# Optimization experiments

Measured on AMD Instinct MI355X. Metric: run time of the kernel, lower is better.

## Reference

```python
import jax, jax.numpy as jnp
import numpy as np

LN_EPS = 1e-5
WINDOWS = (5, 10, 20)


def _rolling_vol_mean(returns, w):
    # returns: [B, L]; rolling unbiased std (torch.std, ddof=1) over window w,
    # then mean over all window positions -> [B, 1]
    B = returns.shape[0]
    z = jnp.zeros((B, 1), returns.dtype)
    c1 = jnp.concatenate([z, jnp.cumsum(returns, axis=1)], axis=1)
    c2 = jnp.concatenate([z, jnp.cumsum(returns * returns, axis=1)], axis=1)
    s1 = c1[:, w:] - c1[:, :-w]          # window sums      [B, L-w+1]
    s2 = c2[:, w:] - c2[:, :-w]          # window sq sums   [B, L-w+1]
    var = (s2 - s1 * s1 / w) / (w - 1)
    std = jnp.sqrt(jnp.maximum(var, 0.0))
    return jnp.mean(std, axis=1, keepdims=True)


def _layernorm(x, g, b):
    mu = jnp.mean(x, axis=-1, keepdims=True)
    v = jnp.mean((x - mu) ** 2, axis=-1, keepdims=True)
    return (x - mu) / jnp.sqrt(v + LN_EPS) * g + b


def setup_inputs() -> dict:
    key = jax.random.key(0)
    ks = jax.random.split(key, 8)
    B, S, F = 4096, 4096, 1
    input_dim, hidden = 64, 256
    h2 = hidden // 2
    price_series = jax.random.uniform(ks[0], (B, S, F), jnp.float32) + 0.5
    sd = 0.02
    return {
        "price_series": price_series,
        "W1": jax.random.normal(ks[1], (input_dim, h2), jnp.float32) * sd,
        "b1": jnp.zeros((h2,), jnp.float32),
        "g1": jnp.ones((h2,), jnp.float32),
        "be1": jnp.zeros((h2,), jnp.float32),
        "W2": jax.random.normal(ks[2], (h2, h2), jnp.float32) * sd,
        "b2": jnp.zeros((h2,), jnp.float32),
        "g2": jnp.ones((h2,), jnp.float32),
        "be2": jnp.zeros((h2,), jnp.float32),
        "Wc1": jax.random.normal(ks[3], (hidden, 64), jnp.float32) * sd,
        "bc1": jnp.zeros((64,), jnp.float32),
        "Wc2": jax.random.normal(ks[4], (64, 4), jnp.float32) * sd,
        "bc2": jnp.zeros((4,), jnp.float32),
    }


def reference(price_series, W1, b1, g1, be1, W2, b2, g2, be2, Wc1, bc1, Wc2, bc2):
    input_dim = W1.shape[0]
    # features == 1 path: log returns
    safe_prices = jnp.clip(price_series, 1e-8, None)
    log_prices = jnp.log(safe_prices)
    returns = (log_prices[:, 1:, 0] - log_prices[:, :-1, 0])  # [B, S-1]

    vol_feats = [_rolling_vol_mean(returns, w) for w in WINDOWS]
    vol = jnp.concatenate(vol_feats, axis=1)                  # [B, 3]
    B = vol.shape[0]
    pad = jnp.zeros((B, input_dim - vol.shape[1]), vol.dtype)
    vol = jnp.concatenate([vol, pad], axis=1)                 # [B, input_dim]

    h = _layernorm(jax.nn.relu(vol @ W1 + b1), g1, be1)       # [B, h2]
    h2f = _layernorm(jax.nn.relu(h @ W2 + b2), g2, be2)       # [B, h2]
    combined = jnp.concatenate([h, h2f], axis=1)              # [B, hidden]
    logits = jax.nn.relu(combined @ Wc1 + bc1) @ Wc2 + bc2    # dropout = identity at eval
    regime = jax.nn.softmax(logits, axis=1)
    return combined, regime
```

## Files before the change

### kernel.cpp

```cpp
#include <hip/hip_runtime.h>
#include <math.h>

constexpr int S   = 4096;
constexpr int L   = S - 1;
constexpr int H2  = 128;
constexpr int HID = 256;
constexpr int NPOS = 16;
constexpr int WMAX = 20;
constexpr int RMAX = NPOS + WMAX - 1;
constexpr float LN_EPS = 1e-5f;

constexpr int LP4 = 1040;

__device__ __forceinline__ float fast_sqrt(float x)  { return __builtin_amdgcn_sqrtf(x); }
__device__ __forceinline__ float fast_rsqrt(float x) { return __builtin_amdgcn_rsqf(x); }

__device__ __forceinline__ int swz(int slot) { return slot ^ ((slot >> 2) & 3); }

__device__ __forceinline__ float2 block_sum2(float a, float b, int tid, float* red8) {
    #pragma unroll
    for (int off = 32; off; off >>= 1) {
        a += __shfl_down(a, off);
        b += __shfl_down(b, off);
    }
    if ((tid & 63) == 0) { red8[(tid >> 6) * 2] = a; red8[(tid >> 6) * 2 + 1] = b; }
    __syncthreads();
    float2 r = make_float2(red8[0] + red8[2] + red8[4] + red8[6],
                           red8[1] + red8[3] + red8[5] + red8[7]);
    __syncthreads();
    return r;
}

template<int W>
__device__ __forceinline__ float window_acc(const float (&rr)[RMAX], int t0,
                                            float s1, float s2) {
    constexpr float c1 = 1.f / (float)(W - 1);
    constexpr float c2 = 1.f / ((float)W * (float)(W - 1));
    const int n = L - W + 1;
    float acc = 0.f;
    #pragma unroll
    for (int i = 0; i < NPOS; ++i) {
        float t  = fmaf(-(s1 * c2), s1, s2 * c1);
        float sd = fast_sqrt(fmaxf(t, 0.f));
        if (t0 + i < n) acc += sd;
        if (i < NPOS - 1) {
            float xin = rr[i + W], xout = rr[i];
            s1 += xin; s1 -= xout;
            s2 = fmaf(xin, xin, s2);
            s2 = fmaf(-xout, xout, s2);
        }
    }
    return acc;
}

__global__ __launch_bounds__(256)
void vol_fused(const float* __restrict__ prices,
               const float* __restrict__ W1,  const float* __restrict__ b1,
               const float* __restrict__ g1,  const float* __restrict__ be1,
               const float* __restrict__ W2,  const float* __restrict__ b2,
               const float* __restrict__ g2,  const float* __restrict__ be2,
               const float* __restrict__ Wc1, const float* __restrict__ bc1,
               const float* __restrict__ Wc2, const float* __restrict__ bc2,
               float* __restrict__ out_combined, float* __restrict__ out_regime)
{
    __shared__ __align__(16) float4 lp4[LP4];
    __shared__ float redv[16];
    __shared__ float vols[4];

    float* fbuf = reinterpret_cast<float*>(lp4);
    float* comb = fbuf;
    float* part = fbuf + 256;
    float* red8 = fbuf + 1280;

    const int tid = threadIdx.x;
    const int b   = blockIdx.x;

    const float4* prow = reinterpret_cast<const float4*>(prices + (size_t)b * S);
    #pragma unroll
    for (int i = 0; i < 4; ++i) {
        int slot = tid + i * 256;
        float4 v = prow[slot];
        float4 w;
        w.x = __logf(fmaxf(v.x, 1e-8f));
        w.y = __logf(fmaxf(v.y, 1e-8f));
        w.z = __logf(fmaxf(v.z, 1e-8f));
        w.w = __logf(fmaxf(v.w, 1e-8f));
        lp4[swz(slot)] = w;
    }
    if (tid < 16) lp4[swz(1024 + tid)] = make_float4(0.f, 0.f, 0.f, 0.f);
    __syncthreads();

    const int t0 = tid * NPOS;
    const int st = tid * 4;
    float lpv[36];
    #pragma unroll
    for (int j = 0; j < 9; ++j) {
        float4 v = lp4[swz(st + j)];
        lpv[4 * j + 0] = v.x; lpv[4 * j + 1] = v.y;
        lpv[4 * j + 2] = v.z; lpv[4 * j + 3] = v.w;
    }
    float rr[RMAX];
    #pragma unroll
    for (int i = 0; i < RMAX; ++i) rr[i] = lpv[i + 1] - lpv[i];

    float s1a = 0.f, s2a = 0.f;
    #pragma unroll
    for (int j = 0; j < 5; ++j) { s1a += rr[j]; s2a = fmaf(rr[j], rr[j], s2a); }
    float s1b = s1a, s2b = s2a;
    #pragma unroll
    for (int j = 5; j < 10; ++j) { s1b += rr[j]; s2b = fmaf(rr[j], rr[j], s2b); }
    float s1c = s1b, s2c = s2b;
    #pragma unroll
    for (int j = 10; j < 20; ++j) { s1c += rr[j]; s2c = fmaf(rr[j], rr[j], s2c); }

    float sum5  = window_acc<5>(rr, t0, s1a, s2a);
    float sum10 = window_acc<10>(rr, t0, s1b, s2b);
    float sum20 = window_acc<20>(rr, t0, s1c, s2c);

    #pragma unroll
    for (int off = 32; off; off >>= 1) {
        sum5  += __shfl_down(sum5,  off);
        sum10 += __shfl_down(sum10, off);
        sum20 += __shfl_down(sum20, off);
    }
    if ((tid & 63) == 0) {
        int w = tid >> 6;
        redv[w * 3 + 0] = sum5; redv[w * 3 + 1] = sum10; redv[w * 3 + 2] = sum20;
    }
    __syncthreads();
    if (tid < 3) {
        constexpr float sc[3] = { 1.f / (L - 5 + 1), 1.f / (L - 10 + 1), 1.f / (L - 20 + 1) };
        vols[tid] = (redv[tid] + redv[3 + tid] + redv[6 + tid] + redv[9 + tid]) * sc[tid];
    }
    __syncthreads();

    const float v0 = vols[0], v1 = vols[1], v2 = vols[2];

    float x = 0.f;
    if (tid < H2) {
        x = b1[tid];
        x = fmaf(v0, W1[0 * H2 + tid], x);
        x = fmaf(v1, W1[1 * H2 + tid], x);
        x = fmaf(v2, W1[2 * H2 + tid], x);
        x = fmaxf(x, 0.f);
    }
    float2 s = block_sum2((tid < H2) ? x : 0.f, (tid < H2) ? x * x : 0.f, tid, red8);
    {
        float mu  = s.x * (1.f / H2);
        float var = s.y * (1.f / H2) - mu * mu;
        if (tid < H2)
            comb[tid] = (x - mu) * fast_rsqrt(fmaxf(var, 0.f) + LN_EPS) * g1[tid] + be1[tid];
    }
    __syncthreads();

    {
        const int q = tid & 31, seg = tid >> 5;
        const float* w2base = W2 + (size_t)(seg * 16) * H2 + q * 4;
        float ax = 0.f, ay = 0.f, az = 0.f, aw = 0.f;
        #pragma unroll
        for (int k = 0; k < 16; ++k) {
            float a = comb[seg * 16 + k];
            float4 w = *reinterpret_cast<const float4*>(w2base + (size_t)k * H2);
            ax = fmaf(a, w.x, ax); ay = fmaf(a, w.y, ay);
            az = fmaf(a, w.z, az); aw = fmaf(a, w.w, aw);
        }
        float4* p4 = reinterpret_cast<float4*>(part);
        p4[tid] = make_float4(ax, ay, az, aw);
    }
    __syncthreads();
    float x2 = 0.f;
    if (tid < H2) {
        float ssum = 0.f;
        #pragma unroll
        for (int sg = 0; sg < 8; ++sg) ssum += part[sg * 128 + tid];
        x2 = fmaxf(ssum + b2[tid], 0.f);
    }
    s = block_sum2((tid < H2) ? x2 : 0.f, (tid < H2) ? x2 * x2 : 0.f, tid, red8);
    {
        float mu  = s.x * (1.f / H2);
        float var = s.y * (1.f / H2) - mu * mu;
        if (tid < H2)
            comb[H2 + tid] = (x2 - mu) * fast_rsqrt(fmaxf(var, 0.f) + LN_EPS) * g2[tid] + be2[tid];
    }
    __syncthreads();

    out_combined[(size_t)b * HID + tid] = comb[tid];

    {
        const int q = tid & 15, seg = tid >> 4;
        const float* wcbase = Wc1 + (size_t)(seg * 16) * 64 + q * 4;
        float ax = 0.f, ay = 0.f, az = 0.f, aw = 0.f;
        #pragma unroll
        for (int k = 0; k < 16; ++k) {
            float a = comb[seg * 16 + k];
            float4 w = *reinterpret_cast<const float4*>(wcbase + (size_t)k * 64);
            ax = fmaf(a, w.x, ax); ay = fmaf(a, w.y, ay);
            az = fmaf(a, w.z, az); aw = fmaf(a, w.w, aw);
        }
        float4* p4 = reinterpret_cast<float4*>(part);
        p4[tid] = make_float4(ax, ay, az, aw);
    }
    __syncthreads();

    if (tid < 64) {
        float ssum = 0.f;
        #pragma unroll
        for (int sg = 0; sg < 16; ++sg) ssum += part[sg * 64 + tid];
        float c1 = fmaxf(ssum + bc1[tid], 0.f);

        float4 wrow = reinterpret_cast<const float4*>(Wc2)[tid];
        float lx = c1 * wrow.x, ly = c1 * wrow.y, lz = c1 * wrow.z, lw = c1 * wrow.w;
        #pragma unroll
        for (int off = 32; off; off >>= 1) {
            lx += __shfl_down(lx, off);
            ly += __shfl_down(ly, off);
            lz += __shfl_down(lz, off);
            lw += __shfl_down(lw, off);
        }
        if (tid == 0) {
            float4 bb = *reinterpret_cast<const float4*>(bc2);
            float l0 = lx + bb.x, l1 = ly + bb.y, l2 = lz + bb.z, l3 = lw + bb.w;
            float m  = fmaxf(fmaxf(l0, l1), fmaxf(l2, l3));
            float e0 = __expf(l0 - m), e1 = __expf(l1 - m);
            float e2 = __expf(l2 - m), e3 = __expf(l3 - m);
            float inv = 1.f / (e0 + e1 + e2 + e3);
            reinterpret_cast<float4*>(out_regime)[b] =
                make_float4(e0 * inv, e1 * inv, e2 * inv, e3 * inv);
        }
    }
}

extern "C" void kernel_launch(void* const* d_in, const int* in_sizes, int n_in,
                              void* d_out, int out_size, void* d_ws, size_t ws_size,
                              hipStream_t stream) {
    const float* prices = (const float*)d_in[0];
    const float* W1  = (const float*)d_in[1];
    const float* b1  = (const float*)d_in[2];
    const float* g1  = (const float*)d_in[3];
    const float* be1 = (const float*)d_in[4];
    const float* W2  = (const float*)d_in[5];
    const float* b2  = (const float*)d_in[6];
    const float* g2  = (const float*)d_in[7];
    const float* be2 = (const float*)d_in[8];
    const float* Wc1 = (const float*)d_in[9];
    const float* bc1 = (const float*)d_in[10];
    const float* Wc2 = (const float*)d_in[11];
    const float* bc2 = (const float*)d_in[12];

    const int B = in_sizes[0] / S;
    float* out_combined = (float*)d_out;
    float* out_regime   = (float*)d_out + (size_t)B * HID;

    vol_fused<<<B, 256, 0, stream>>>(prices, W1, b1, g1, be1, W2, b2, g2, be2,
                                     Wc1, bc1, Wc2, bc2, out_combined, out_regime);
}
```

Baseline: 43.65 us.

## Split fused kernel into vol-stats and 4-row batched MLP kernels

Splits the single per-row kernel into two launches. The first computes the rolling volatility stats per row and writes them to workspace. The second runs the MLP/LayerNorm/softmax over 4 rows per block, so each weight load is reused across 4 rows and each block has fewer barrier-bound serial phases. It also drops the LDS swizzle in favor of a linear layout, and adds a fast path without the bounds check for interior windows. In exchange it pays for a second kernel launch and a small workspace round-trip, and the unswizzled LDS reads may hit bank conflicts.

Measured after the change: 49.00 us. 12.3% more time.

```diff
diff --git a/kernel.cpp b/kernel.cpp
--- a/kernel.cpp
+++ b/kernel.cpp
@@ -10,26 +10,8 @@
 constexpr int RMAX = NPOS + WMAX - 1;
 constexpr float LN_EPS = 1e-5f;
 
-constexpr int LP4 = 1040;
-
 __device__ __forceinline__ float fast_sqrt(float x)  { return __builtin_amdgcn_sqrtf(x); }
 __device__ __forceinline__ float fast_rsqrt(float x) { return __builtin_amdgcn_rsqf(x); }
-
-__device__ __forceinline__ int swz(int slot) { return slot ^ ((slot >> 2) & 3); }
-
-__device__ __forceinline__ float2 block_sum2(float a, float b, int tid, float* red8) {
-    #pragma unroll
-    for (int off = 32; off; off >>= 1) {
-        a += __shfl_down(a, off);
-        b += __shfl_down(b, off);
-    }
-    if ((tid & 63) == 0) { red8[(tid >> 6) * 2] = a; red8[(tid >> 6) * 2 + 1] = b; }
-    __syncthreads();
-    float2 r = make_float2(red8[0] + red8[2] + red8[4] + red8[6],
-                           red8[1] + red8[3] + red8[5] + red8[7]);
-    __syncthreads();
-    return r;
-}
 
 template<int W>
 __device__ __forceinline__ float window_acc(const float (&rr)[RMAX], int t0,
@@ -38,23 +20,103 @@
     constexpr float c2 = 1.f / ((float)W * (float)(W - 1));
     const int n = L - W + 1;
     float acc = 0.f;
-    #pragma unroll
-    for (int i = 0; i < NPOS; ++i) {
-        float t  = fmaf(-(s1 * c2), s1, s2 * c1);
-        float sd = fast_sqrt(fmaxf(t, 0.f));
-        if (t0 + i < n) acc += sd;
-        if (i < NPOS - 1) {
-            float xin = rr[i + W], xout = rr[i];
-            s1 += xin; s1 -= xout;
-            s2 = fmaf(xin, xin, s2);
-            s2 = fmaf(-xout, xout, s2);
+    if (t0 + NPOS <= n) {
+        #pragma unroll
+        for (int i = 0; i < NPOS; ++i) {
+            float t = fmaf(-(s1 * c2), s1, s2 * c1);
+            acc += fast_sqrt(fmaxf(t, 0.f));
+            if (i < NPOS - 1) {
+                float xin = rr[i + W], xout = rr[i];
+                s1 += xin; s1 -= xout;
+                s2 = fmaf(xin, xin, s2);
+                s2 = fmaf(-xout, xout, s2);
+            }
+        }
+    } else {
+        #pragma unroll
+        for (int i = 0; i < NPOS; ++i) {
+            float t  = fmaf(-(s1 * c2), s1, s2 * c1);
+            float sd = fast_sqrt(fmaxf(t, 0.f));
+            if (t0 + i < n) acc += sd;
+            if (i < NPOS - 1) {
+                float xin = rr[i + W], xout = rr[i];
+                s1 += xin; s1 -= xout;
+                s2 = fmaf(xin, xin, s2);
+                s2 = fmaf(-xout, xout, s2);
+            }
         }
     }
     return acc;
 }
 
 __global__ __launch_bounds__(256)
-void vol_fused(const float* __restrict__ prices,
+void vol_stats(const float* __restrict__ prices, float* __restrict__ vols_out)
+{
+    __shared__ __align__(16) float lp[S + 40];
+    __shared__ float redv[16];
+
+    const int tid = threadIdx.x;
+    const int b   = blockIdx.x;
+
+    const float4* prow = reinterpret_cast<const float4*>(prices + (size_t)b * S);
+    #pragma unroll
+    for (int i = 0; i < 4; ++i) {
+        int idx = tid + i * 256;
+        float4 v = prow[idx];
+        lp[idx * 4 + 0] = __logf(fmaxf(v.x, 1e-8f));
+        lp[idx * 4 + 1] = __logf(fmaxf(v.y, 1e-8f));
+        lp[idx * 4 + 2] = __logf(fmaxf(v.z, 1e-8f));
+        lp[idx * 4 + 3] = __logf(fmaxf(v.w, 1e-8f));
+    }
+    if (tid < 40) lp[S + tid] = 0.f;
+    __syncthreads();
+
+    const int t0 = tid * NPOS;
+    float lpv[36];
+    #pragma unroll
+    for (int j = 0; j < 9; ++j) {
+        float4 v = *reinterpret_cast<const float4*>(&lp[t0 + 4 * j]);
+        lpv[4 * j + 0] = v.x; lpv[4 * j + 1] = v.y;
+        lpv[4 * j + 2] = v.z; lpv[4 * j + 3] = v.w;
+    }
+    float rr[RMAX];
+    #pragma unroll
+    for (int i = 0; i < RMAX; ++i) rr[i] = lpv[i + 1] - lpv[i];
+
+    float s1a = 0.f, s2a = 0.f;
+    #pragma unroll
+    for (int j = 0; j < 5; ++j)  { s1a += rr[j]; s2a = fmaf(rr[j], rr[j], s2a); }
+    float s1b = s1a, s2b = s2a;
+    #pragma unroll
+    for (int j = 5; j < 10; ++j) { s1b += rr[j]; s2b = fmaf(rr[j], rr[j], s2b); }
+    float s1c = s1b, s2c = s2b;
+    #pragma unroll
+    for (int j = 10; j < 20; ++j){ s1c += rr[j]; s2c = fmaf(rr[j], rr[j], s2c); }
+
+    float sum5  = window_acc<5>(rr, t0, s1a, s2a);
+    float sum10 = window_acc<10>(rr, t0, s1b, s2b);
+    float sum20 = window_acc<20>(rr, t0, s1c, s2c);
+
+    #pragma unroll
+    for (int off = 32; off; off >>= 1) {
+        sum5  += __shfl_down(sum5,  off);
+        sum10 += __shfl_down(sum10, off);
+        sum20 += __shfl_down(sum20, off);
+    }
+    if ((tid & 63) == 0) {
+        int w = tid >> 6;
+        redv[w * 3 + 0] = sum5; redv[w * 3 + 1] = sum10; redv[w * 3 + 2] = sum20;
+    }
+    __syncthreads();
+    if (tid < 3) {
+        constexpr float sc[3] = { 1.f / (L - 5 + 1), 1.f / (L - 10 + 1), 1.f / (L - 20 + 1) };
+        vols_out[b * 4 + tid] =
+            (redv[tid] + redv[3 + tid] + redv[6 + tid] + redv[9 + tid]) * sc[tid];
+    }
+}
+
+__global__ __launch_bounds__(256)
+void mlp_batch(const float* __restrict__ vols,
                const float* __restrict__ W1,  const float* __restrict__ b1,
                const float* __restrict__ g1,  const float* __restrict__ be1,
                const float* __restrict__ W2,  const float* __restrict__ b2,
@@ -63,170 +125,145 @@
                const float* __restrict__ Wc2, const float* __restrict__ bc2,
                float* __restrict__ out_combined, float* __restrict__ out_regime)
 {
-    __shared__ __align__(16) float4 lp4[LP4];
-    __shared__ float redv[16];
-    __shared__ float vols[4];
-
-    float* fbuf = reinterpret_cast<float*>(lp4);
-    float* comb = fbuf;
-    float* part = fbuf + 256;
-    float* red8 = fbuf + 1280;
+    __shared__ float comb[4][HID];
+    __shared__ __align__(16) float partb[1024];
+    __shared__ float c1s[4][64];
+    __shared__ float2 musig[4];
+    __shared__ float lgt[16];
+    __shared__ __align__(16) float vls[4][4];
 
     const int tid = threadIdx.x;
-    const int b   = blockIdx.x;
-
-    const float4* prow = reinterpret_cast<const float4*>(prices + (size_t)b * S);
-    #pragma unroll
-    for (int i = 0; i < 4; ++i) {
-        int slot = tid + i * 256;
-        float4 v = prow[slot];
-        float4 w;
-        w.x = __logf(fmaxf(v.x, 1e-8f));
-        w.y = __logf(fmaxf(v.y, 1e-8f));
-        w.z = __logf(fmaxf(v.z, 1e-8f));
-        w.w = __logf(fmaxf(v.w, 1e-8f));
-        lp4[swz(slot)] = w;
-    }
-    if (tid < 16) lp4[swz(1024 + tid)] = make_float4(0.f, 0.f, 0.f, 0.f);
-    __syncthreads();
-
-    const int t0 = tid * NPOS;
-    const int st = tid * 4;
-    float lpv[36];
-    #pragma unroll
-    for (int j = 0; j < 9; ++j) {
-        float4 v = lp4[swz(st + j)];
-        lpv[4 * j + 0] = v.x; lpv[4 * j + 1] = v.y;
-        lpv[4 * j + 2] = v.z; lpv[4 * j + 3] = v.w;
-    }
-    float rr[RMAX];
-    #pragma unroll
-    for (int i = 0; i < RMAX; ++i) rr[i] = lpv[i + 1] - lpv[i];
-
-    float s1a = 0.f, s2a = 0.f;
-    #pragma unroll
-    for (int j = 0; j < 5; ++j) { s1a += rr[j]; s2a = fmaf(rr[j], rr[j], s2a); }
-    float s1b = s1a, s2b = s2a;
-    #pragma unroll
-    for (int j = 5; j < 10; ++j) { s1b += rr[j]; s2b = fmaf(rr[j], rr[j], s2b); }
-    float s1c = s1b, s2c = s2b;
-    #pragma unroll
-    for (int j = 10; j < 20; ++j) { s1c += rr[j]; s2c = fmaf(rr[j], rr[j], s2c); }
-
-    float sum5  = window_acc<5>(rr, t0, s1a, s2a);
-    float sum10 = window_acc<10>(rr, t0, s1b, s2b);
-    float sum20 = window_acc<20>(rr, t0, s1c, s2c);
-
-    #pragma unroll
-    for (int off = 32; off; off >>= 1) {
-        sum5  += __shfl_down(sum5,  off);
-        sum10 += __shfl_down(sum10, off);
-        sum20 += __shfl_down(sum20, off);
-    }
-    if ((tid & 63) == 0) {
-        int w = tid >> 6;
-        redv[w * 3 + 0] = sum5; redv[w * 3 + 1] = sum10; redv[w * 3 + 2] = sum20;
-    }
-    __syncthreads();
-    if (tid < 3) {
-        constexpr float sc[3] = { 1.f / (L - 5 + 1), 1.f / (L - 10 + 1), 1.f / (L - 20 + 1) };
-        vols[tid] = (redv[tid] + redv[3 + tid] + redv[6 + tid] + redv[9 + tid]) * sc[tid];
-    }
-    __syncthreads();
-
-    const float v0 = vols[0], v1 = vols[1], v2 = vols[2];
-
-    float x = 0.f;
-    if (tid < H2) {
-        x = b1[tid];
-        x = fmaf(v0, W1[0 * H2 + tid], x);
-        x = fmaf(v1, W1[1 * H2 + tid], x);
-        x = fmaf(v2, W1[2 * H2 + tid], x);
-        x = fmaxf(x, 0.f);
-    }
-    float2 s = block_sum2((tid < H2) ? x : 0.f, (tid < H2) ? x * x : 0.f, tid, red8);
-    {
-        float mu  = s.x * (1.f / H2);
-        float var = s.y * (1.f / H2) - mu * mu;
-        if (tid < H2)
-            comb[tid] = (x - mu) * fast_rsqrt(fmaxf(var, 0.f) + LN_EPS) * g1[tid] + be1[tid];
-    }
-    __syncthreads();
-
-    {
-        const int q = tid & 31, seg = tid >> 5;
-        const float* w2base = W2 + (size_t)(seg * 16) * H2 + q * 4;
+    const int r0  = blockIdx.x * 4;
+
+    if (tid < 4)
+        *reinterpret_cast<float4*>(vls[tid]) =
+            reinterpret_cast<const float4*>(vols)[r0 + tid];
+    __syncthreads();
+
+    const int c  = tid & 127;
+    const int r2 = tid >> 7;
+    const float w0 = W1[c], w1 = W1[H2 + c], w2 = W1[2 * H2 + c];
+    const float bb1 = b1[c], gg1 = g1[c], ee1 = be1[c];
+    float xa = fmaxf(fmaf(vls[r2][2],   w2, fmaf(vls[r2][1],   w1, fmaf(vls[r2][0],   w0, bb1))), 0.f);
+    float xb = fmaxf(fmaf(vls[r2+2][2], w2, fmaf(vls[r2+2][1], w1, fmaf(vls[r2+2][0], w0, bb1))), 0.f);
+    comb[r2][c] = xa; comb[r2 + 2][c] = xb;
+    __syncthreads();
+    {
+        const int r = tid >> 6, lane = tid & 63;
+        float2 v = *reinterpret_cast<const float2*>(&comb[r][lane * 2]);
+        float s = v.x + v.y, sq = v.x * v.x + v.y * v.y;
+        #pragma unroll
+        for (int off = 32; off; off >>= 1) { s += __shfl_down(s, off); sq += __shfl_down(sq, off); }
+        if (lane == 0) {
+            float mu = s * (1.f / H2);
+            float var = sq * (1.f / H2) - mu * mu;
+            musig[r] = make_float2(mu, fast_rsqrt(fmaxf(var, 0.f) + LN_EPS));
+        }
+    }
+    __syncthreads();
+    {
+        float2 ma = musig[r2], mb = musig[r2 + 2];
+        comb[r2][c]     = (xa - ma.x) * ma.y * gg1 + ee1;
+        comb[r2 + 2][c] = (xb - mb.x) * mb.y * gg1 + ee1;
+    }
+    __syncthreads();
+
+    {
+        const int q = tid & 31, r = (tid >> 5) & 3, h = tid >> 7;
+        const float* wb = W2 + (size_t)(h * 64) * H2 + q * 4;
         float ax = 0.f, ay = 0.f, az = 0.f, aw = 0.f;
-        #pragma unroll
-        for (int k = 0; k < 16; ++k) {
-            float a = comb[seg * 16 + k];
-            float4 w = *reinterpret_cast<const float4*>(w2base + (size_t)k * H2);
+        #pragma unroll 8
+        for (int k = 0; k < 64; ++k) {
+            float a = comb[r][h * 64 + k];
+            float4 w = *reinterpret_cast<const float4*>(wb + (size_t)k * H2);
             ax = fmaf(a, w.x, ax); ay = fmaf(a, w.y, ay);
             az = fmaf(a, w.z, az); aw = fmaf(a, w.w, aw);
         }
-        float4* p4 = reinterpret_cast<float4*>(part);
-        p4[tid] = make_float4(ax, ay, az, aw);
-    }
-    __syncthreads();
-    float x2 = 0.f;
-    if (tid < H2) {
-        float ssum = 0.f;
-        #pragma unroll
-        for (int sg = 0; sg < 8; ++sg) ssum += part[sg * 128 + tid];
-        x2 = fmaxf(ssum + b2[tid], 0.f);
-    }
-    s = block_sum2((tid < H2) ? x2 : 0.f, (tid < H2) ? x2 * x2 : 0.f, tid, red8);
-    {
-        float mu  = s.x * (1.f / H2);
-        float var = s.y * (1.f / H2) - mu * mu;
-        if (tid < H2)
-            comb[H2 + tid] = (x2 - mu) * fast_rsqrt(fmaxf(var, 0.f) + LN_EPS) * g2[tid] + be2[tid];
-    }
-    __syncthreads();
-
-    out_combined[(size_t)b * HID + tid] = comb[tid];
-
-    {
-        const int q = tid & 15, seg = tid >> 4;
-        const float* wcbase = Wc1 + (size_t)(seg * 16) * 64 + q * 4;
+        reinterpret_cast<float4*>(partb)[tid] = make_float4(ax, ay, az, aw);
+    }
+    __syncthreads();
+    float ya, yb;
+    {
+        const int qq = c >> 2, cc = c & 3;
+        ya = fmaxf(partb[(0 * 128 + r2 * 32 + qq) * 4 + cc] +
+                   partb[(1 * 128 + r2 * 32 + qq) * 4 + cc] + b2[c], 0.f);
+        yb = fmaxf(partb[(0 * 128 + (r2 + 2) * 32 + qq) * 4 + cc] +
+                   partb[(1 * 128 + (r2 + 2) * 32 + qq) * 4 + cc] + b2[c], 0.f);
+        comb[r2][H2 + c] = ya; comb[r2 + 2][H2 + c] = yb;
+    }
+    __syncthreads();
+    {
+        const int r = tid >> 6, lane = tid & 63;
+        float2 v = *reinterpret_cast<const float2*>(&comb[r][H2 + lane * 2]);
+        float s = v.x + v.y, sq = v.x * v.x + v.y * v.y;
+        #pragma unroll
+        for (int off = 32; off; off >>= 1) { s += __shfl_down(s, off); sq += __shfl_down(sq, off); }
+        if (lane == 0) {
+            float mu = s * (1.f / H2);
+            float var = sq * (1.f / H2) - mu * mu;
+            musig[r] = make_float2(mu, fast_rsqrt(fmaxf(var, 0.f) + LN_EPS));
+        }
+    }
+    __syncthreads();
+    {
+        const float gg2 = g2[c], ee2 = be2[c];
+        float2 ma = musig[r2], mb = musig[r2 + 2];
+        comb[r2][H2 + c]     = (ya - ma.x) * ma.y * gg2 + ee2;
+        comb[r2 + 2][H2 + c] = (yb - mb.x) * mb.y * gg2 + ee2;
+    }
+    __syncthreads();
+
+    {
+        const int cq = tid & 15, r = (tid >> 4) & 3, qt = tid >> 6;
+        const float* wb = Wc1 + (size_t)(qt * 64) * 64 + cq * 4;
         float ax = 0.f, ay = 0.f, az = 0.f, aw = 0.f;
-        #pragma unroll
-        for (int k = 0; k < 16; ++k) {
-            float a = comb[seg * 16 + k];
-            float4 w = *reinterpret_cast<const float4*>(wcbase + (size_t)k * 64);
+        #pragma unroll 8
+        for (int k = 0; k < 64; ++k) {
+            float a = comb[r][qt * 64 + k];
+            float4 w = *reinterpret_cast<const float4*>(wb + (size_t)k * 64);
             ax = fmaf(a, w.x, ax); ay = fmaf(a, w.y, ay);
             az = fmaf(a, w.z, az); aw = fmaf(a, w.w, aw);
         }
-        float4* p4 = reinterpret_cast<float4*>(part);
-        p4[tid] = make_float4(ax, ay, az, aw);
+        reinterpret_cast<float4*>(partb)[tid] = make_float4(ax, ay, az, aw);
+    }
+    __syncthreads();
+    {
+        const int cc = tid & 63, r = tid >> 6;
+        const int cq = cc >> 2, ci = cc & 3;
+        float ssum = partb[(0 * 64 + r * 16 + cq) * 4 + ci] +
+                     partb[(1 * 64 + r * 16 + cq) * 4 + ci] +
+                     partb[(2 * 64 + r * 16 + cq) * 4 + ci] +
+                     partb[(3 * 64 + r * 16 + cq) * 4 + ci];
+        c1s[r][cc] = fmaxf(ssum + bc1[cc], 0.f);
     }
     __syncthreads();
 
     if (tid < 64) {
-        float ssum = 0.f;
-        #pragma unroll
-        for (int sg = 0; sg < 16; ++sg) ssum += part[sg * 64 + tid];
-        float c1 = fmaxf(ssum + bc1[tid], 0.f);
-
-        float4 wrow = reinterpret_cast<const float4*>(Wc2)[tid];
-        float lx = c1 * wrow.x, ly = c1 * wrow.y, lz = c1 * wrow.z, lw = c1 * wrow.w;
-        #pragma unroll
-        for (int off = 32; off; off >>= 1) {
-            lx += __shfl_down(lx, off);
-            ly += __shfl_down(ly, off);
-            lz += __shfl_down(lz, off);
-            lw += __shfl_down(lw, off);
-        }
-        if (tid == 0) {
-            float4 bb = *reinterpret_cast<const float4*>(bc2);
-            float l0 = lx + bb.x, l1 = ly + bb.y, l2 = lz + bb.z, l3 = lw + bb.w;
-            float m  = fmaxf(fmaxf(l0, l1), fmaxf(l2, l3));
-            float e0 = __expf(l0 - m), e1 = __expf(l1 - m);
-            float e2 = __expf(l2 - m), e3 = __expf(l3 - m);
-            float inv = 1.f / (e0 + e1 + e2 + e3);
-            reinterpret_cast<float4*>(out_regime)[b] =
-                make_float4(e0 * inv, e1 * inv, e2 * inv, e3 * inv);
-        }
+        const int j = tid & 3, r = (tid >> 2) & 3, q4 = tid >> 4;
+        float p = 0.f;
+        #pragma unroll
+        for (int k = 0; k < 16; ++k)
+            p = fmaf(c1s[r][q4 * 16 + k], Wc2[(q4 * 16 + k) * 4 + j], p);
+        p += __shfl_down(p, 32);
+        p += __shfl_down(p, 16);
+        if (tid < 16) lgt[tid] = p + bc2[j];
+    }
+    __syncthreads();
+    if (tid < 4) {
+        float l0 = lgt[tid * 4 + 0], l1 = lgt[tid * 4 + 1];
+        float l2 = lgt[tid * 4 + 2], l3 = lgt[tid * 4 + 3];
+        float m  = fmaxf(fmaxf(l0, l1), fmaxf(l2, l3));
+        float e0 = __expf(l0 - m), e1 = __expf(l1 - m);
+        float e2 = __expf(l2 - m), e3 = __expf(l3 - m);
+        float inv = 1.f / (e0 + e1 + e2 + e3);
+        reinterpret_cast<float4*>(out_regime)[r0 + tid] =
+            make_float4(e0 * inv, e1 * inv, e2 * inv, e3 * inv);
+    }
+
+    {
+        const int r = tid >> 6, c4 = tid & 63;
+        float4 v = *reinterpret_cast<const float4*>(&comb[r][c4 * 4]);
+        reinterpret_cast<float4*>(out_combined)[(size_t)(r0 + r) * 64 + c4] = v;
     }
 }
 
@@ -250,7 +287,9 @@
     const int B = in_sizes[0] / S;
     float* out_combined = (float*)d_out;
     float* out_regime   = (float*)d_out + (size_t)B * HID;
-
-    vol_fused<<<B, 256, 0, stream>>>(prices, W1, b1, g1, be1, W2, b2, g2, be2,
-                                     Wc1, bc1, Wc2, bc2, out_combined, out_regime);
-}
+    float* vols_ws      = (float*)d_ws;
+
+    vol_stats<<<B, 256, 0, stream>>>(prices, vols_ws);
+    mlp_batch<<<B / 4, 256, 0, stream>>>(vols_ws, W1, b1, g1, be1, W2, b2, g2, be2,
+                                         Wc1, bc1, Wc2, bc2, out_combined, out_regime);
+}
```
